# Kernel tuning notes

Measured on AMD Instinct MI355X. Metric: run time of the kernel, lower is better.

Reference implementation:

```python
import math
import jax, jax.numpy as jnp
import numpy as np

B, T, D, H, E, K = 2, 2048, 1024, 16, 8, 2
HD = D // H                      # head_dim = 64
CAP = math.ceil(1.25 * B * T / E)  # capacity per expert = 640
NEG = -1e9


def setup_inputs() -> dict:
    key = jax.random.key(0)
    ks = jax.random.split(key, 8)
    s = 0.02
    return {
        "x": jax.random.normal(ks[0], (B, T, D), jnp.float32),
        "ln1_g": jnp.ones((D,), jnp.float32),
        "ln1_b": jnp.zeros((D,), jnp.float32),
        "w_qkv": jax.random.normal(ks[1], (3 * D, D), jnp.float32) * s,
        "w_proj": jax.random.normal(ks[2], (D, D), jnp.float32) * s,
        "ln2_g": jnp.ones((D,), jnp.float32),
        "ln2_b": jnp.zeros((D,), jnp.float32),
        "w_gate": jax.random.normal(ks[3], (E, D), jnp.float32) * s,
        "w1": jax.random.normal(ks[4], (E, D, 4 * D), jnp.float32) * s,
        "b1": jnp.zeros((E, 4 * D), jnp.float32),
        "w2": jax.random.normal(ks[5], (E, 4 * D, D), jnp.float32) * s,
        "b2": jnp.zeros((E, D), jnp.float32),
    }


def _layernorm(x, g, b, eps=1e-5):
    m = x.mean(-1, keepdims=True)
    v = ((x - m) ** 2).mean(-1, keepdims=True)
    return (x - m) * jax.lax.rsqrt(v + eps) * g + b


def _rope(q, k):
    # q,k: [B,T,H,HD]; rotate-half RoPE with half_dim = HD//2 frequencies
    half = HD // 2
    pos = jnp.arange(T, dtype=jnp.float32)[:, None]
    inv_freq = 1.0 / (10000.0 ** (jnp.arange(0, HD, 2, dtype=jnp.float32) / HD))
    ang = pos * inv_freq                              # [T, half]
    sin = jnp.sin(ang)[None, :, None, :]
    cos = jnp.cos(ang)[None, :, None, :]

    def rot(t):
        t1, t2 = t[..., :half], t[..., half:]
        return jnp.concatenate([t1 * cos - t2 * sin, t1 * sin + t2 * cos], -1)

    return rot(q), rot(k)


def _attention(x, w_qkv, w_proj):
    qkv = (x @ w_qkv.T).reshape(B, T, H, 3 * HD)
    q, k, v = jnp.split(qkv, 3, axis=-1)              # each [B,T,H,HD]
    q, k = _rope(q, k)
    scores = jnp.einsum('bqhd,bkhd->bhqk', q, k) / math.sqrt(HD)
    causal = jnp.tril(jnp.ones((T, T), bool))
    scores = jnp.where(causal, scores, NEG)
    probs = jax.nn.softmax(scores, axis=-1)
    out = jnp.einsum('bhqk,bkhd->bqhd', probs, v).reshape(B, T, D)
    return out @ w_proj.T


def _sparse_moe(x2d, w_gate, w1, b1, w2, b2):
    # x2d: [N, D] flattened tokens. Eval mode: no noise, no dropout.
    N = x2d.shape[0]
    gates = jax.nn.softmax((x2d @ w_gate.T).astype(jnp.float32), axis=-1)  # [N,E]
    gate_vals, idx = jax.lax.top_k(gates, K)          # [N,K]
    gate_vals = gate_vals.astype(x2d.dtype)

    # Capacity enforcement: token order position within each expert
    mask = jnp.zeros((N, E), bool).at[jnp.arange(N)[:, None], idx].set(True)
    pos = jnp.cumsum(mask.astype(jnp.int32), axis=0) * mask - 1   # [N,E]
    keep = (pos < CAP) & mask
    slot = jnp.take_along_axis(pos, idx, axis=1)      # [N,K]
    kept = jnp.take_along_axis(keep, idx, axis=1)     # [N,K] bool

    # Dispatch: dropped tokens go to pad slot CAP (masked out at combine)
    slot_w = jnp.where(kept, slot, CAP).reshape(-1)   # [N*K]
    e_flat = idx.reshape(-1)                          # [N*K]
    xk = jnp.broadcast_to(x2d[:, None, :], (N, K, D)).reshape(-1, D)
    xk = xk * kept.reshape(-1, 1)
    buf = jnp.zeros((E, CAP + 1, D), x2d.dtype).at[e_flat, slot_w].set(xk)

    # Grouped expert MLP (GELU exact, matching nn.GELU default)
    h = jax.nn.gelu(jnp.einsum('ecd,edf->ecf', buf, w1) + b1[:, None, :],
                    approximate=False)
    out = jnp.einsum('ecf,efd->ecd', h, w2) + b2[:, None, :]

    # Combine: gather each token's expert output, weight by gate, mask drops
    y = out[e_flat, slot_w].reshape(N, K, D) * (gate_vals * kept)[..., None]
    return y.sum(axis=1)


def reference(x, ln1_g, ln1_b, w_qkv, w_proj, ln2_g, ln2_b,
              w_gate, w1, b1, w2, b2):
    h = x + _attention(_layernorm(x, ln1_g, ln1_b), w_qkv, w_proj)
    moe_in = _layernorm(h, ln2_g, ln2_b)
    moe_out = _sparse_moe(moe_in.reshape(B * T, D), w_gate, w1, b1, w2, b2)
    return h + moe_out.reshape(B, T, D)
```

## Files before the change

kernel.cpp:

```cpp
#include <hip/hip_runtime.h>
#include <hip/hip_bf16.h>

typedef __bf16 bf16;
typedef __attribute__((ext_vector_type(8))) __bf16 bf16x8;
typedef __attribute__((ext_vector_type(4))) __bf16 bf16x4;
typedef __attribute__((ext_vector_type(4))) float f32x4;
typedef __attribute__((ext_vector_type(16))) float f32x16;

#define NB 2
#define NT 2048
#define ND 1024
#define NH 16
#define HD_ 64
#define NE 8
#define NCAP 640
#define NTOK 4096
#define NDFF 4096

static __device__ __forceinline__ f32x4 mfma16(bf16x8 a, bf16x8 b, f32x4 c) {
  return __builtin_amdgcn_mfma_f32_16x16x32_bf16(a, b, c, 0, 0, 0);
}
static __device__ __forceinline__ f32x16 mfma32(bf16x8 a, bf16x8 b, f32x16 c) {
  return __builtin_amdgcn_mfma_f32_32x32x16_bf16(a, b, c, 0, 0, 0);
}
static __device__ __forceinline__ unsigned pk2(float a, float b) {
  union { __bf16 h[2]; unsigned u; } z;
  z.h[0] = (__bf16)a; z.h[1] = (__bf16)b;
  return z.u;
}
static __device__ __forceinline__ void gload_lds16(const bf16* g, bf16* l) {
  __builtin_amdgcn_global_load_lds(
      (const __attribute__((address_space(1))) unsigned int*)g,
      (__attribute__((address_space(3))) unsigned int*)l, 16, 0, 0);
}

__global__ __launch_bounds__(256) void cvt_k(const float* __restrict__ in,
                                             bf16* __restrict__ out, int n4) {
  int i = blockIdx.x * 256 + threadIdx.x;
  int stride = gridDim.x * 256;
  for (; i < n4; i += stride) {
    f32x4 v = ((const f32x4*)in)[i];
    bf16x4 o;
    o[0] = (bf16)v[0]; o[1] = (bf16)v[1]; o[2] = (bf16)v[2]; o[3] = (bf16)v[3];
    ((bf16x4*)out)[i] = o;
  }
}

__global__ __launch_bounds__(256) void transpose_k(const float* __restrict__ in,
                                                   bf16* __restrict__ out, int R, int C) {
  __shared__ float tile[64][65];
  const size_t zoff = (size_t)blockIdx.z * R * C;
  in += zoff; out += zoff;
  const int c0 = blockIdx.x * 64, r0 = blockIdx.y * 64;
  const int tx = threadIdx.x & 15, ty = threadIdx.x >> 4;
#pragma unroll
  for (int i = 0; i < 4; i++) {
    const int r = i * 16 + ty;
    f32x4 v = *(const f32x4*)(in + (size_t)(r0 + r) * C + c0 + tx * 4);
    *(f32x4*)&tile[r][tx * 4] = v;
  }
  __syncthreads();
#pragma unroll
  for (int i = 0; i < 4; i++) {
    const int rr = i * 16 + ty;
    bf16x4 o;
#pragma unroll
    for (int j = 0; j < 4; j++) o[j] = (bf16)tile[tx * 4 + j][rr];
    *(bf16x4*)(out + (size_t)(c0 + rr) * R + r0 + tx * 4) = o;
  }
}

__global__ __launch_bounds__(256) void transpose_v_k(const bf16* __restrict__ v,
                                                     bf16* __restrict__ vT) {
  __shared__ bf16 tile[32][33];
  int bh = blockIdx.z;
  const bf16* in = v + (size_t)bh * NT * HD_;
  bf16* out = vT + (size_t)bh * HD_ * NT;
  int t0 = blockIdx.x * 32, d0 = blockIdx.y * 32;
  int tx = threadIdx.x, ty = threadIdx.y;
#pragma unroll
  for (int i = 0; i < 4; i++)
    tile[ty + i * 8][tx] = in[(size_t)(t0 + ty + i * 8) * HD_ + d0 + tx];
  __syncthreads();
#pragma unroll
  for (int i = 0; i < 4; i++)
    out[(size_t)(d0 + ty + i * 8) * NT + t0 + tx] = tile[tx][ty + i * 8];
}

__global__ void rope_tab_k(float* __restrict__ tab) {
  int t = blockIdx.x, i = threadIdx.x;
  float inv = powf(10000.f, -(float)(2 * i) * (1.f / 64.f));
  float ang = (float)t * inv;
  float s, c;
  sincosf(ang, &s, &c);
  tab[(t * 32 + i) * 2] = s;
  tab[(t * 32 + i) * 2 + 1] = c;
}

template <bool BF16OUT>
__global__ __launch_bounds__(256) void ln_k(const float* __restrict__ in,
                                            const float* __restrict__ g,
                                            const float* __restrict__ bb,
                                            bf16* __restrict__ outb,
                                            float* __restrict__ outf) {
  const int row = blockIdx.x;
  const float* xr = in + (size_t)row * ND;
  const int tid = threadIdx.x, lane = tid & 63, wid = tid >> 6;
  f32x4 v = ((const f32x4*)xr)[tid];
  float s = v[0] + v[1] + v[2] + v[3];
  float sq = v[0] * v[0] + v[1] * v[1] + v[2] * v[2] + v[3] * v[3];
#pragma unroll
  for (int m = 1; m < 64; m <<= 1) {
    s += __shfl_xor(s, m, 64);
    sq += __shfl_xor(sq, m, 64);
  }
  __shared__ float red[8];
  if (lane == 0) { red[wid] = s; red[4 + wid] = sq; }
  __syncthreads();
  s = red[0] + red[1] + red[2] + red[3];
  sq = red[4] + red[5] + red[6] + red[7];
  float mean = s * (1.f / 1024.f);
  float var = sq * (1.f / 1024.f) - mean * mean;
  float rs = rsqrtf(var + 1e-5f);
#pragma unroll
  for (int c = 0; c < 4; c++) {
    int col = tid * 4 + c;
    float y = (v[c] - mean) * rs * g[col] + bb[col];
    if constexpr (BF16OUT) outb[(size_t)row * ND + col] = (bf16)y;
    else outf[(size_t)row * ND + col] = y;
  }
}

#define EPI_SPLIT_QKV 0
#define EPI_ADD_X 1
#define EPI_BIAS_GELU 2
#define EPI_STORE 3

template <int EPI, int STAGE>
__global__ __launch_bounds__(256) void gemm_bt_k(
    const bf16* __restrict__ A, const bf16* __restrict__ Bw,
    const int M, const int N, const int K,
    const size_t zA, const size_t zB, const size_t zOut, const size_t zBias,
    const float* __restrict__ bias, const float* __restrict__ Xadd,
    void* __restrict__ Out, bf16* __restrict__ k_out, bf16* __restrict__ v_out) {
  const int z = blockIdx.z;
  const int m0 = blockIdx.y * 128, n0 = blockIdx.x * 128;
  const int tid = threadIdx.x, lane = tid & 63, wid = tid >> 6;
  const int wm = (wid >> 1) * 64, wn = (wid & 1) * 64;
  const int l15 = lane & 15, ksl = lane >> 4;
  const int nst = K / 64;
  constexpr int LDB = (STAGE == 1) ? 72 : 64;
  __shared__ __align__(16) bf16 As[128 * LDB];
  __shared__ __align__(16) bf16 Bs[128 * LDB];
  f32x4 acc[4][4];
#pragma unroll
  for (int i = 0; i < 4; i++)
#pragma unroll
    for (int j = 0; j < 4; j++) acc[i][j] = (f32x4){0.f, 0.f, 0.f, 0.f};

  if constexpr (STAGE == 0) {
    const int lr = lane >> 3, lc = (lane & 7) * 8;
    const bf16* Ag = A + zA * z + (size_t)(m0 + wid * 32 + lr) * K + lc;
    const bf16* Bg = Bw + zB * z + (size_t)(n0 + wid * 32 + lr) * K + lc;
    for (int s = 0; s < nst; ++s) {
      __syncthreads();
#pragma unroll
      for (int it = 0; it < 4; it++) {
        gload_lds16(Ag + (size_t)(it * 8) * K + s * 64, &As[(wid * 32 + it * 8) * 64]);
        gload_lds16(Bg + (size_t)(it * 8) * K + s * 64, &Bs[(wid * 32 + it * 8) * 64]);
      }
      __syncthreads();
#pragma unroll
      for (int kk = 0; kk < 2; kk++) {
        bf16x8 af[4], bfr[4];
        const int ko = kk * 32 + ksl * 8;
#pragma unroll
        for (int i = 0; i < 4; i++)
          af[i] = *(const bf16x8*)&As[(wm + i * 16 + l15) * 64 + ko];
#pragma unroll
        for (int j = 0; j < 4; j++)
          bfr[j] = *(const bf16x8*)&Bs[(wn + j * 16 + l15) * 64 + ko];
#pragma unroll
        for (int i = 0; i < 4; i++)
#pragma unroll
          for (int j = 0; j < 4; j++)
            acc[i][j] = mfma16(af[i], bfr[j], acc[i][j]);
      }
    }
  } else {
    const int sr = tid >> 3, sc = (tid & 7) * 8;
    const bf16* Ag = A + zA * z + (size_t)(m0 + sr) * K + sc;
    const bf16* Bg = Bw + zB * z + (size_t)(n0 + sr) * K + sc;
    bf16x8 av[4], bv[4];
#pragma unroll
    for (int it = 0; it < 4; it++) {
      av[it] = *(const bf16x8*)(Ag + (size_t)(it * 32) * K);
      bv[it] = *(const bf16x8*)(Bg + (size_t)(it * 32) * K);
    }
    for (int s = 0; s < nst; ++s) {
      __syncthreads();
#pragma unroll
      for (int it = 0; it < 4; it++) {
        *(bf16x8*)&As[(sr + it * 32) * LDB + sc] = av[it];
        *(bf16x8*)&Bs[(sr + it * 32) * LDB + sc] = bv[it];
      }
      __syncthreads();
      if (s + 1 < nst) {
#pragma unroll
        for (int it = 0; it < 4; it++) {
          av[it] = *(const bf16x8*)(Ag + (size_t)(it * 32) * K + (s + 1) * 64);
          bv[it] = *(const bf16x8*)(Bg + (size_t)(it * 32) * K + (s + 1) * 64);
        }
      }
#pragma unroll
      for (int kk = 0; kk < 2; kk++) {
        bf16x8 af[4], bfr[4];
        const int ko = kk * 32 + ksl * 8;
#pragma unroll
        for (int i = 0; i < 4; i++)
          af[i] = *(const bf16x8*)&As[(wm + i * 16 + l15) * LDB + ko];
#pragma unroll
        for (int j = 0; j < 4; j++)
          bfr[j] = *(const bf16x8*)&Bs[(wn + j * 16 + l15) * LDB + ko];
#pragma unroll
        for (int i = 0; i < 4; i++)
#pragma unroll
          for (int j = 0; j < 4; j++)
            acc[i][j] = mfma16(af[i], bfr[j], acc[i][j]);
      }
    }
  }

#pragma unroll
  for (int i = 0; i < 4; i++) {
#pragma unroll
    for (int j = 0; j < 4; j++) {
      const int mb = m0 + wm + i * 16 + ksl * 4;
      const int nc = n0 + wn + j * 16 + l15;
#pragma unroll
      for (int r = 0; r < 4; r++) {
        const int mr = mb + r;
        float vacc = acc[i][j][r];
        if constexpr (EPI == EPI_SPLIT_QKV) {
          const int h = nc / 192;
          const int rr = nc - h * 192;
          const int which = rr >> 6;
          const int d = rr & 63;
          const int b = mr >> 11, t = mr & 2047;
          bf16* dst = (which == 0) ? (bf16*)Out : (which == 1 ? k_out : v_out);
          dst[(((size_t)(b * NH + h)) * NT + t) * HD_ + d] = (bf16)vacc;
        } else if constexpr (EPI == EPI_ADD_X) {
          ((float*)Out)[(size_t)mr * N + nc] = vacc + Xadd[(size_t)mr * N + nc];
        } else if constexpr (EPI == EPI_BIAS_GELU) {
          float x = vacc + bias[zBias * z + nc];
          float gl = 0.5f * x * (1.f + erff(x * 0.70710678118654752f));
          ((bf16*)Out)[zOut * z + (size_t)mr * N + nc] = (bf16)gl;
        } else {
          ((bf16*)Out)[zOut * z + (size_t)mr * N + nc] = (bf16)vacc;
        }
      }
    }
  }
}

__global__ __launch_bounds__(256) void rope_k(bf16* __restrict__ q, bf16* __restrict__ k,
                                              const float* __restrict__ tab) {
  const int bh = blockIdx.y;
  const int t = blockIdx.x * 4 + (threadIdx.x >> 6);
  const int d = threadIdx.x & 63;
  const size_t row = ((size_t)bh * NT + t) * HD_;
  const int i = d & 31;
  const float sn = tab[(t * 32 + i) * 2], cs = tab[(t * 32 + i) * 2 + 1];
  {
    float a = (float)q[row + d];
    float b2 = (float)q[row + (d ^ 32)];
    float o = (d < 32) ? (a * cs - b2 * sn) : (b2 * sn + a * cs);
    q[row + d] = (bf16)(o * 0.18033688011112042f);
  }
  {
    float a = (float)k[row + d];
    float b2 = (float)k[row + (d ^ 32)];
    float o = (d < 32) ? (a * cs - b2 * sn) : (b2 * sn + a * cs);
    k[row + d] = (bf16)o;
  }
}

__global__ __launch_bounds__(256) void attn_k(const bf16* __restrict__ q,
                                              const bf16* __restrict__ k,
                                              const bf16* __restrict__ vT,
                                              bf16* __restrict__ attn_out) {
  __shared__ __align__(16) bf16 Kt[64 * 64];
  __shared__ __align__(16) bf16 Vt[64 * 64];
  const int bid = blockIdx.x;
  const int bh = bid & 31;
  const int ti = (bid >> 5) & 7;
  const int qt = (bid >> 8) ? (15 - ti) : ti;
  const int q0 = qt * 128;
  const int tid = threadIdx.x, lane = tid & 63, wid = tid >> 6;
  const int l31 = lane & 31, hi = lane >> 5;
  const int q0w = q0 + wid * 32;
  const int qrow = q0w + l31;
  const size_t base = (size_t)bh * (NT * HD_);
  const size_t baseT = (size_t)bh * (HD_ * NT);

  bf16x8 qf[4];
#pragma unroll
  for (int ks = 0; ks < 4; ks++)
    qf[ks] = *(const bf16x8*)(q + base + (size_t)qrow * HD_ + ks * 16 + hi * 8);

  f32x16 ot0, ot1;
#pragma unroll
  for (int r = 0; r < 16; r++) { ot0[r] = 0.f; ot1[r] = 0.f; }
  float m2 = -1e30f, l = 0.f;

  const int ntiles = qt * 2 + 2;
  const int swz = (l31 & 7);
  for (int t = 0; t < ntiles; t++) {
    const int kv0 = t * 64;
    __syncthreads();
#pragma unroll
    for (int rr = 0; rr < 2; rr++) {
      int f = rr * 256 + tid;
      int row = f >> 3, c = f & 7;
      int cw = ((c ^ (row & 7)) * 8);
      *(bf16x8*)&Kt[row * 64 + cw] =
          *(const bf16x8*)(k + base + (size_t)(kv0 + row) * HD_ + c * 8);
      *(bf16x8*)&Vt[row * 64 + cw] =
          *(const bf16x8*)(vT + baseT + (size_t)row * NT + kv0 + c * 8);
    }
    __syncthreads();
    if (kv0 > q0w + 31) continue;

    f32x16 s0, s1;
#pragma unroll
    for (int r = 0; r < 16; r++) { s0[r] = 0.f; s1[r] = 0.f; }
#pragma unroll
    for (int ks = 0; ks < 4; ks++) {
      const int cw = (((ks * 2 + hi) ^ swz) * 8);
      bf16x8 ka0 = *(const bf16x8*)&Kt[l31 * 64 + cw];
      bf16x8 ka1 = *(const bf16x8*)&Kt[(l31 + 32) * 64 + cw];
      s0 = mfma32(ka0, qf[ks], s0);
      s1 = mfma32(ka1, qf[ks], s1);
    }

    float p[32];
#pragma unroll
    for (int r = 0; r < 16; r++) { p[r] = s0[r]; p[16 + r] = s1[r]; }
    if (kv0 + 63 > q0w) {
#pragma unroll
      for (int sub = 0; sub < 2; sub++)
#pragma unroll
        for (int r = 0; r < 16; r++) {
          int kvg = kv0 + sub * 32 + (r & 3) + 8 * (r >> 2) + 4 * hi;
          if (kvg > qrow) p[sub * 16 + r] = -1e30f;
        }
    }
    float tm = p[0];
#pragma unroll
    for (int r = 1; r < 32; r++) tm = fmaxf(tm, p[r]);
    tm = fmaxf(tm, __shfl_xor(tm, 32, 64));
    float mn = fmaxf(m2, tm);
    float sf = exp2f(m2 - mn);
    m2 = mn;
    float ts = 0.f;
#pragma unroll
    for (int r = 0; r < 32; r++) { p[r] = exp2f(p[r] - mn); ts += p[r]; }
    ts += __shfl_xor(ts, 32, 64);
    l = l * sf + ts;
#pragma unroll
    for (int r = 0; r < 16; r++) { ot0[r] *= sf; ot1[r] *= sf; }

#pragma unroll
    for (int ks = 0; ks < 4; ks++) {
      const int i0 = (ks >> 1) * 16 + (ks & 1) * 8;
      unsigned Aw = pk2(p[i0 + 0], p[i0 + 1]);
      unsigned Bw = pk2(p[i0 + 2], p[i0 + 3]);
      unsigned Cw = pk2(p[i0 + 4], p[i0 + 5]);
      unsigned Dw = pk2(p[i0 + 6], p[i0 + 7]);
      unsigned xA = (unsigned)__shfl_xor((int)Aw, 32, 64);
      unsigned xB = (unsigned)__shfl_xor((int)Bw, 32, 64);
      unsigned xC = (unsigned)__shfl_xor((int)Cw, 32, 64);
      unsigned xD = (unsigned)__shfl_xor((int)Dw, 32, 64);
      union { unsigned u[4]; bf16x8 v; } pa;
      pa.u[0] = hi ? xC : Aw;
      pa.u[1] = hi ? xD : Bw;
      pa.u[2] = hi ? Cw : xA;
      pa.u[3] = hi ? Dw : xB;
      const int cw = (((ks * 2 + hi) ^ swz) * 8);
      bf16x8 va0 = *(const bf16x8*)&Vt[l31 * 64 + cw];
      bf16x8 va1 = *(const bf16x8*)&Vt[(l31 + 32) * 64 + cw];
      ot0 = mfma32(va0, pa.v, ot0);
      ot1 = mfma32(va1, pa.v, ot1);
    }
  }

  const int b = bh >> 4, h = bh & 15;
  const float inv = 1.f / l;
  const size_t orow = ((size_t)(b * NT + qrow)) * ND + h * 64;
#pragma unroll
  for (int g = 0; g < 4; g++) {
    bf16x4 w0, w1;
#pragma unroll
    for (int c = 0; c < 4; c++) {
      w0[c] = (bf16)(ot0[g * 4 + c] * inv);
      w1[c] = (bf16)(ot1[g * 4 + c] * inv);
    }
    *(bf16x4*)(attn_out + orow + g * 8 + 4 * hi) = w0;
    *(bf16x4*)(attn_out + orow + 32 + g * 8 + 4 * hi) = w1;
  }
}

__global__ __launch_bounds__(256) void gate_k(const float* __restrict__ moe_in,
                                              const float* __restrict__ w_gate,
                                              int* __restrict__ idx, float* __restrict__ gv) {
  __shared__ float wg[8 * 1024];
  for (int i = threadIdx.x; i < 8192; i += 256) wg[i] = w_gate[i];
  __syncthreads();
  const int lane = threadIdx.x & 63, wid = threadIdx.x >> 6;
  for (int tt = 0; tt < 4; tt++) {
    const int n = blockIdx.x * 16 + wid * 4 + tt;
    const float* xr = moe_in + (size_t)n * ND;
    float a[8];
#pragma unroll
    for (int e = 0; e < 8; e++) a[e] = 0.f;
    for (int d0 = lane * 4; d0 < 1024; d0 += 256) {
      f32x4 xv = *(const f32x4*)(xr + d0);
#pragma unroll
      for (int e = 0; e < 8; e++) {
        const float* wr = &wg[e * 1024 + d0];
        a[e] += xv[0] * wr[0] + xv[1] * wr[1] + xv[2] * wr[2] + xv[3] * wr[3];
      }
    }
#pragma unroll
    for (int e = 0; e < 8; e++)
#pragma unroll
      for (int m = 1; m < 64; m <<= 1) a[e] += __shfl_xor(a[e], m, 64);
    if (lane == 0) {
      float mx = a[0];
#pragma unroll
      for (int e = 1; e < 8; e++) mx = fmaxf(mx, a[e]);
      float p[8], se = 0.f;
#pragma unroll
      for (int e = 0; e < 8; e++) { p[e] = expf(a[e] - mx); se += p[e]; }
      float inv = 1.f / se;
#pragma unroll
      for (int e = 0; e < 8; e++) p[e] *= inv;
      int i1 = 0; float v1 = p[0];
#pragma unroll
      for (int e = 1; e < 8; e++) if (p[e] > v1) { v1 = p[e]; i1 = e; }
      int i2 = -1; float v2 = -1.f;
#pragma unroll
      for (int e = 0; e < 8; e++) if (e != i1 && p[e] > v2) { v2 = p[e]; i2 = e; }
      idx[n * 2] = i1; idx[n * 2 + 1] = i2;
      gv[n * 2] = v1; gv[n * 2 + 1] = v2;
    }
  }
}

__global__ void scan_k(const int* __restrict__ idx, int* __restrict__ slot,
                       int* __restrict__ kept) {
  const int lane = threadIdx.x;
  int base[8];
#pragma unroll
  for (int e = 0; e < 8; e++) base[e] = 0;
  const unsigned long long lm = (lane == 63) ? ~0ull : ((1ull << (lane + 1)) - 1);
  for (int c = 0; c < 64; c++) {
    const int n = c * 64 + lane;
    const int e0 = idx[n * 2], e1 = idx[n * 2 + 1];
    int s0 = 0, s1 = 0;
#pragma unroll
    for (int e = 0; e < 8; e++) {
      unsigned long long m0 = __ballot(e0 == e);
      unsigned long long m1 = __ballot(e1 == e);
      unsigned long long m = m0 | m1;
      int pref = __popcll(m & lm);
      if (e0 == e) s0 = base[e] + pref - 1;
      if (e1 == e) s1 = base[e] + pref - 1;
      base[e] += __popcll(m);
    }
    slot[n * 2] = s0; slot[n * 2 + 1] = s1;
    kept[n * 2] = (s0 < NCAP) ? 1 : 0;
    kept[n * 2 + 1] = (s1 < NCAP) ? 1 : 0;
  }
}

__global__ __launch_bounds__(64) void scatter_k(const float* __restrict__ moe_in,
                                                const int* __restrict__ idx,
                                                const int* __restrict__ slot,
                                                const int* __restrict__ kept,
                                                bf16* __restrict__ buf) {
  const int a = blockIdx.x;
  if (!kept[a]) return;
  const int n = a >> 1;
  const int e = idx[a], s = slot[a];
  const float* src = moe_in + (size_t)n * ND;
  bf16* dst = buf + ((size_t)e * NCAP + s) * ND;
  for (int c = threadIdx.x * 4; c < 1024; c += 256) {
    f32x4 v = *(const f32x4*)(src + c);
    bf16x4 o;
    o[0] = (bf16)v[0]; o[1] = (bf16)v[1]; o[2] = (bf16)v[2]; o[3] = (bf16)v[3];
    *(bf16x4*)(dst + c) = o;
  }
}

__global__ __launch_bounds__(256) void gather_k(const float* __restrict__ h,
                                                const bf16* __restrict__ eout,
                                                const int* __restrict__ idx,
                                                const int* __restrict__ slot,
                                                const int* __restrict__ kept,
                                                const float* __restrict__ gv,
                                                const float* __restrict__ b2,
                                                float* __restrict__ out) {
  const int n = blockIdx.x;
  const int k0 = kept[n * 2], k1 = kept[n * 2 + 1];
  const int i0 = idx[n * 2], i1 = idx[n * 2 + 1];
  const float g0 = k0 ? gv[n * 2] : 0.f;
  const float g1 = k1 ? gv[n * 2 + 1] : 0.f;
  const size_t r0 = k0 ? ((size_t)i0 * NCAP + slot[n * 2]) * ND : 0;
  const size_t r1 = k1 ? ((size_t)i1 * NCAP + slot[n * 2 + 1]) * ND : 0;
  const int c = threadIdx.x * 4;
  f32x4 o = *(const f32x4*)(h + (size_t)n * ND + c);
  if (k0) {
    bf16x4 e = *(const bf16x4*)(eout + r0 + c);
    f32x4 bb = *(const f32x4*)(b2 + i0 * ND + c);
#pragma unroll
    for (int cc = 0; cc < 4; cc++) o[cc] += g0 * ((float)e[cc] + bb[cc]);
  }
  if (k1) {
    bf16x4 e = *(const bf16x4*)(eout + r1 + c);
    f32x4 bb = *(const f32x4*)(b2 + i1 * ND + c);
#pragma unroll
    for (int cc = 0; cc < 4; cc++) o[cc] += g1 * ((float)e[cc] + bb[cc]);
  }
  *(f32x4*)(out + (size_t)n * ND + c) = o;
}

extern "C" void kernel_launch(void* const* d_in, const int* in_sizes, int n_in,
                              void* d_out, int out_size, void* d_ws, size_t ws_size,
                              hipStream_t stream) {
  (void)in_sizes; (void)n_in; (void)out_size;
  const float* x      = (const float*)d_in[0];
  const float* ln1_g  = (const float*)d_in[1];
  const float* ln1_b  = (const float*)d_in[2];
  const float* w_qkv  = (const float*)d_in[3];
  const float* w_proj = (const float*)d_in[4];
  const float* ln2_g  = (const float*)d_in[5];
  const float* ln2_b  = (const float*)d_in[6];
  const float* w_gate = (const float*)d_in[7];
  const float* w1     = (const float*)d_in[8];
  const float* b1     = (const float*)d_in[9];
  const float* w2     = (const float*)d_in[10];
  const float* b2     = (const float*)d_in[11];
  float* out = (float*)d_out;

  char* ws = (char*)d_ws;
  size_t off = 0;
  auto alloc = [&](size_t bytes) -> char* {
    char* p = ws + off;
    off += (bytes + 255) & ~(size_t)255;
    return p;
  };
  bf16* w1t    = (bf16*)alloc((size_t)NE * NDFF * ND * 2);
  bf16* w2t    = (bf16*)alloc((size_t)NE * ND * NDFF * 2);
  bf16* wqkvb  = (bf16*)alloc((size_t)3 * ND * ND * 2);
  bf16* wprojb = (bf16*)alloc((size_t)ND * ND * 2);
  float* hbufr = (float*)alloc((size_t)NTOK * ND * 4);
  float* moein = (float*)alloc((size_t)NTOK * ND * 4);
  float* ropet = (float*)alloc((size_t)NT * 32 * 2 * 4);
  int*   idx   = (int*)alloc((size_t)NTOK * 2 * 4);
  int*   slot  = (int*)alloc((size_t)NTOK * 2 * 4);
  int*   kept  = (int*)alloc((size_t)NTOK * 2 * 4);
  float* gv    = (float*)alloc((size_t)NTOK * 2 * 4);
  char*  S     = alloc((size_t)62914560);
  if (off > ws_size) return;

  const size_t MB8 = (size_t)8388608;
  bf16* xn    = (bf16*)(S);
  bf16* qp    = (bf16*)(S + MB8);
  bf16* kp    = (bf16*)(S + 2 * MB8);
  bf16* vp    = (bf16*)(S + 3 * MB8);
  bf16* attnp = (bf16*)(S + 4 * MB8);
  bf16* vTp   = (bf16*)(S);
  bf16* hbuf  = (bf16*)(S);
  bf16* buf   = (bf16*)(S + (size_t)41943040);
  bf16* eout  = (bf16*)(S + (size_t)52428800);

  dim3 tb(32, 8);
  cvt_k<<<2048, 256, 0, stream>>>(w_qkv, wqkvb, 3 * ND * ND / 4);
  cvt_k<<<1024, 256, 0, stream>>>(w_proj, wprojb, ND * ND / 4);
  transpose_k<<<dim3(NDFF / 64, ND / 64, NE), 256, 0, stream>>>(w1, w1t, ND, NDFF);
  transpose_k<<<dim3(ND / 64, NDFF / 64, NE), 256, 0, stream>>>(w2, w2t, NDFF, ND);
  rope_tab_k<<<NT, 32, 0, stream>>>(ropet);
  ln_k<true><<<NTOK, 256, 0, stream>>>(x, ln1_g, ln1_b, xn, nullptr);
  gemm_bt_k<EPI_SPLIT_QKV, 0><<<dim3(3 * ND / 128, NTOK / 128, 1), 256, 0, stream>>>(
      xn, wqkvb, NTOK, 3 * ND, ND, 0, 0, 0, 0, nullptr, nullptr, qp, kp, vp);
  transpose_v_k<<<dim3(NT / 32, HD_ / 32, NB * NH), tb, 0, stream>>>(vp, vTp);
  rope_k<<<dim3(NT / 4, NB * NH), 256, 0, stream>>>(qp, kp, ropet);
  attn_k<<<512, 256, 0, stream>>>(qp, kp, vTp, attnp);
  gemm_bt_k<EPI_ADD_X, 1><<<dim3(ND / 128, NTOK / 128, 1), 256, 0, stream>>>(
      attnp, wprojb, NTOK, ND, ND, 0, 0, 0, 0, nullptr, x, hbufr, nullptr, nullptr);
  ln_k<false><<<NTOK, 256, 0, stream>>>(hbufr, ln2_g, ln2_b, nullptr, moein);
  gate_k<<<NTOK / 16, 256, 0, stream>>>(moein, w_gate, idx, gv);
  scan_k<<<1, 64, 0, stream>>>(idx, slot, kept);
  scatter_k<<<NTOK * 2, 64, 0, stream>>>(moein, idx, slot, kept, buf);
  gemm_bt_k<EPI_BIAS_GELU, 0><<<dim3(NDFF / 128, NCAP / 128, NE), 256, 0, stream>>>(
      buf, w1t, NCAP, NDFF, ND, (size_t)NCAP * ND, (size_t)NDFF * ND,
      (size_t)NCAP * NDFF, NDFF, b1, nullptr, hbuf, nullptr, nullptr);
  gemm_bt_k<EPI_STORE, 1><<<dim3(ND / 128, NCAP / 128, NE), 256, 0, stream>>>(
      hbuf, w2t, NCAP, ND, NDFF, (size_t)NCAP * NDFF, (size_t)ND * NDFF,
      (size_t)NCAP * ND, 0, nullptr, nullptr, eout, nullptr, nullptr);
  gather_k<<<NTOK, 256, 0, stream>>>(hbufr, eout, idx, slot, kept, gv, b2, out);
}
```

Before: 487.9 us.

## Prefetch next K/V tile into registers and skip lazy softmax rescale

The attention kernel now loads the next K and V tile from global memory into registers while the current tile is being computed, then writes those registers to shared memory at the top of the next iteration. This hides global-load latency behind the MFMA and softmax work. It also adds a lazy online-softmax rescale: the running max and the output accumulators are only updated when some row's new max exceeds the old one by more than 8 (in log2 units). The prefetch uses more registers, and the lazy rescale lets exponentials grow up to 2^8 before renormalising, which stays safe in fp32.

```diff
diff --git a/kernel.cpp b/kernel.cpp
--- a/kernel.cpp
+++ b/kernel.cpp
@@ -315,20 +315,32 @@
 
   const int ntiles = qt * 2 + 2;
   const int swz = (l31 & 7);
+  const int strow = tid >> 3, stc = tid & 7;
+  const int cw0 = ((stc ^ (strow & 7)) * 8);
+  bf16x8 kr[2], vr[2];
+#pragma unroll
+  for (int rr = 0; rr < 2; rr++) {
+    kr[rr] = *(const bf16x8*)(k + base + (size_t)(strow + rr * 32) * HD_ + stc * 8);
+    vr[rr] = *(const bf16x8*)(vT + baseT + (size_t)(strow + rr * 32) * NT + stc * 8);
+  }
+
   for (int t = 0; t < ntiles; t++) {
     const int kv0 = t * 64;
     __syncthreads();
 #pragma unroll
     for (int rr = 0; rr < 2; rr++) {
-      int f = rr * 256 + tid;
-      int row = f >> 3, c = f & 7;
-      int cw = ((c ^ (row & 7)) * 8);
-      *(bf16x8*)&Kt[row * 64 + cw] =
-          *(const bf16x8*)(k + base + (size_t)(kv0 + row) * HD_ + c * 8);
-      *(bf16x8*)&Vt[row * 64 + cw] =
-          *(const bf16x8*)(vT + baseT + (size_t)row * NT + kv0 + c * 8);
+      *(bf16x8*)&Kt[(strow + rr * 32) * 64 + cw0] = kr[rr];
+      *(bf16x8*)&Vt[(strow + rr * 32) * 64 + cw0] = vr[rr];
     }
     __syncthreads();
+    if (t + 1 < ntiles) {
+      const int kn = kv0 + 64;
+#pragma unroll
+      for (int rr = 0; rr < 2; rr++) {
+        kr[rr] = *(const bf16x8*)(k + base + (size_t)(kn + strow + rr * 32) * HD_ + stc * 8);
+        vr[rr] = *(const bf16x8*)(vT + baseT + (size_t)(strow + rr * 32) * NT + kn + stc * 8);
+      }
+    }
     if (kv0 > q0w + 31) continue;
 
     f32x16 s0, s1;
@@ -359,16 +371,19 @@
 #pragma unroll
     for (int r = 1; r < 32; r++) tm = fmaxf(tm, p[r]);
     tm = fmaxf(tm, __shfl_xor(tm, 32, 64));
-    float mn = fmaxf(m2, tm);
-    float sf = exp2f(m2 - mn);
-    m2 = mn;
+    if (!__all(tm <= m2 + 8.f)) {
+      float mn = fmaxf(m2, tm);
+      float sf = exp2f(m2 - mn);
+      m2 = mn;
+      l *= sf;
+#pragma unroll
+      for (int r = 0; r < 16; r++) { ot0[r] *= sf; ot1[r] *= sf; }
+    }
     float ts = 0.f;
 #pragma unroll
-    for (int r = 0; r < 32; r++) { p[r] = exp2f(p[r] - mn); ts += p[r]; }
+    for (int r = 0; r < 32; r++) { p[r] = exp2f(p[r] - m2); ts += p[r]; }
     ts += __shfl_xor(ts, 32, 64);
-    l = l * sf + ts;
-#pragma unroll
-    for (int r = 0; r < 16; r++) { ot0[r] *= sf; ot1[r] *= sf; }
+    l += ts;
 
 #pragma unroll
     for (int ks = 0; ks < 4; ks++) {
```

Result: faster. 459.1 us (-5.9%).
